# Kernel optimization log

Measured on AMD Instinct MI355X. Metric: run time of the kernel, lower is better.

Reference implementation:

```python
import jax, jax.numpy as jnp
import numpy as np

IN, OUT, RANK = 4096, 4096, 8
ALPHA = 8.0

def _quantize_int8(x):
    # row-wise symmetric int8 quantization (matches torch _quantize_int8)
    scale = jnp.max(jnp.abs(x), axis=1) / 127.0              # [rows]
    q = jnp.round(x / jnp.clip(scale, 1e-12)[:, None]).astype(jnp.int8)
    return q, scale


def setup_inputs() -> dict:
    key = jax.random.key(0)
    k_x, k_w, k_a, k_b = jax.random.split(key, 4)
    x = jax.random.normal(k_x, (8192, IN), dtype=jnp.float32)
    # simulate quantizing a pretrained fp32 weight [OUT, IN]
    w = jax.random.normal(k_w, (OUT, IN), dtype=jnp.float32) * 0.02
    w_scale = jnp.max(jnp.abs(w), axis=1) / 127.0
    weight_i8 = jnp.round(w / jnp.clip(w_scale, 1e-12)[:, None]).astype(jnp.int8)
    weight_scale = w_scale.astype(jnp.float32)               # [OUT]
    # LoRA params (lora_b random instead of zeros so output is nontrivial)
    lora_a = jax.random.normal(k_a, (RANK, IN), dtype=jnp.float32) * (1.0 / np.sqrt(IN))
    lora_b = jax.random.normal(k_b, (OUT, RANK), dtype=jnp.float32) * 0.02
    return {"x": x, "weight_i8": weight_i8, "weight_scale": weight_scale,
            "lora_a": lora_a, "lora_b": lora_b}


def reference(x, weight_i8, weight_scale, lora_a, lora_b):
    # quantize_act=True path: int8 activation quant + int8 GEMM (int32 accum) + dequant
    x_i8, x_scale = _quantize_int8(x)                         # [T, IN] int8, [T]
    out_i32 = jnp.matmul(x_i8, weight_i8.T, preferred_element_type=jnp.int32)  # [T, OUT]
    out = out_i32.astype(jnp.float32) * x_scale[:, None] * weight_scale[None, :]
    # LoRA low-rank add: x @ A^T @ B^T * (alpha / rank)
    out = out + (x @ lora_a.T) @ lora_b.T * (ALPHA / RANK)
    return out
```

## Files before the change

### kernel.cpp

```cpp
#include <hip/hip_runtime.h>
#include <stdint.h>

#define T_DIM   8192
#define IN_DIM  4096
#define OUT_DIM 4096
#define RANK    8

typedef int v4i __attribute__((ext_vector_type(4)));

__device__ __forceinline__ void async_copy16(const void* g, void* l) {
  __builtin_amdgcn_global_load_lds(
      (const __attribute__((address_space(1))) void*)g,
      (__attribute__((address_space(3))) void*)l, 16, 0, 0);
}

#define PW_BLOCKS 16384
#define QX_BLOCKS 8192
#define PREP_BLOCKS (PW_BLOCKS + QX_BLOCKS)

__global__ __launch_bounds__(256) void prep(
    const int* __restrict__ w32,
    const float* __restrict__ x,
    const float* __restrict__ lora_a,
    int8_t* __restrict__ w8,
    int8_t* __restrict__ x_i8,
    float* __restrict__ x_scale,
    float* __restrict__ xa)
{
  const int b = blockIdx.x;
  const int tid = threadIdx.x;
  __shared__ float red[4];
  __shared__ float redx[4][RANK];

  if (b < PW_BLOCKS) {
    const int idx = b * 256 + tid;
    const int4 v = ((const int4*)w32)[idx];
    char4 q;
    q.x = (signed char)v.x; q.y = (signed char)v.y;
    q.z = (signed char)v.z; q.w = (signed char)v.w;
    ((char4*)w8)[idx] = q;
    return;
  }

  const int row = b - PW_BLOCKS;
  const float4* xr = (const float4*)(x + (size_t)row * IN_DIM);
  float4 xv[4];
#pragma unroll
  for (int c = 0; c < 4; ++c) xv[c] = xr[c * 256 + tid];

  float am = 0.f;
#pragma unroll
  for (int c = 0; c < 4; ++c)
    am = fmaxf(am, fmaxf(fmaxf(fabsf(xv[c].x), fabsf(xv[c].y)),
                         fmaxf(fabsf(xv[c].z), fabsf(xv[c].w))));
#pragma unroll
  for (int off = 32; off > 0; off >>= 1)
    am = fmaxf(am, __shfl_xor(am, off, 64));
  if ((tid & 63) == 0) red[tid >> 6] = am;

  float dot[RANK];
#pragma unroll
  for (int r = 0; r < RANK; ++r) {
    const float4* ar = (const float4*)(lora_a + (size_t)r * IN_DIM);
    float s = 0.f;
#pragma unroll
    for (int c = 0; c < 4; ++c) {
      const float4 a = ar[c * 256 + tid];
      s += xv[c].x * a.x + xv[c].y * a.y + xv[c].z * a.z + xv[c].w * a.w;
    }
    dot[r] = s;
  }
#pragma unroll
  for (int off = 32; off > 0; off >>= 1) {
#pragma unroll
    for (int r = 0; r < RANK; ++r)
      dot[r] += __shfl_xor(dot[r], off, 64);
  }
  if ((tid & 63) == 0) {
#pragma unroll
    for (int r = 0; r < RANK; ++r) redx[tid >> 6][r] = dot[r];
  }
  __syncthreads();

  const float amax = fmaxf(fmaxf(red[0], red[1]), fmaxf(red[2], red[3]));
  const float scale = amax * (1.0f / 127.0f);
  const float inv = 1.0f / fmaxf(scale, 1e-12f);
  char4* qout = (char4*)(x_i8 + (size_t)row * IN_DIM);
#pragma unroll
  for (int c = 0; c < 4; ++c) {
    char4 q;
    q.x = (signed char)(int)rintf(xv[c].x * inv);
    q.y = (signed char)(int)rintf(xv[c].y * inv);
    q.z = (signed char)(int)rintf(xv[c].z * inv);
    q.w = (signed char)(int)rintf(xv[c].w * inv);
    qout[c * 256 + tid] = q;
  }
  if (tid == 0) x_scale[row] = scale;
  if (tid < RANK)
    xa[(size_t)row * RANK + tid] =
        redx[0][tid] + redx[1][tid] + redx[2][tid] + redx[3][tid];
}

#define SYNC(n) do {                                      \
    asm volatile("s_waitcnt vmcnt(" #n ")" ::: "memory"); \
    __builtin_amdgcn_s_barrier();                         \
    __builtin_amdgcn_sched_barrier(0);                    \
  } while (0)

__device__ __forceinline__ void stage_tile(const int8_t* aSrc, const int8_t* bSrc,
                                           int8_t* Lbuf, int ldsOff) {
  async_copy16(aSrc,                          Lbuf + ldsOff);
  async_copy16(aSrc + (size_t)128 * IN_DIM,   Lbuf + 8192 + ldsOff);
  async_copy16(bSrc,                          Lbuf + 16384 + ldsOff);
  async_copy16(bSrc + (size_t)128 * IN_DIM,   Lbuf + 16384 + 8192 + ldsOff);
}

__device__ __forceinline__ void compute_tile(const int8_t* Lbuf, int aOff, int bOff,
                                             v4i (&acc)[8][4]) {
  const int8_t* La = Lbuf;
  const int8_t* Lb = Lbuf + 16384;
  v4i aF[8], bF[4];
#pragma unroll
  for (int i = 0; i < 8; ++i) aF[i] = *(const v4i*)(La + aOff + i * 1024);
#pragma unroll
  for (int j = 0; j < 4; ++j) bF[j] = *(const v4i*)(Lb + bOff + j * 1024);
  __builtin_amdgcn_s_setprio(1);
#pragma unroll
  for (int i = 0; i < 8; ++i)
#pragma unroll
    for (int j = 0; j < 4; ++j)
      acc[i][j] = __builtin_amdgcn_mfma_i32_16x16x64_i8(aF[i], bF[j], acc[i][j], 0, 0, 0);
  __builtin_amdgcn_s_setprio(0);
}

__global__ __launch_bounds__(512, 2) void gemm256_i8(
    const int8_t* __restrict__ A,
    const int8_t* __restrict__ B,
    const float* __restrict__ x_scale,
    const float* __restrict__ w_scale,
    const float* __restrict__ xa,
    const float* __restrict__ lora_b,
    float* __restrict__ out)
{
  __shared__ __align__(16) int8_t smem[3 * 32768];
  const int tid = threadIdx.x;

  const int orig = blockIdx.x;
  const int wgid = ((orig & 7) << 6) | (orig >> 3);
  const int by = wgid >> 4;
  const int bx = wgid & 15;
  const size_t arow0 = (size_t)by * 256;
  const size_t brow0 = (size_t)bx * 256;

  const int r_l = tid >> 2;
  const int qsw = ((tid & 3) ^ ((r_l >> 1) & 3)) << 4;
  const int8_t* aSrc = A + (arow0 + r_l) * IN_DIM + qsw;
  const int8_t* bSrc = B + (brow0 + r_l) * IN_DIM + qsw;
  const int ldsOff = tid << 4;

  const int lane = tid & 63;
  const int wave = tid >> 6;
  const int wr = wave >> 2, wc = wave & 3;
  const int m16 = lane & 15, quad = lane >> 4;
  const int sw = (quad ^ ((m16 >> 1) & 3)) << 4;
  const int aOff = (wr * 128 + m16) * 64 + sw;
  const int bOff = (wc * 64 + m16) * 64 + sw;

  v4i acc[8][4];
  const v4i vz = {0, 0, 0, 0};
#pragma unroll
  for (int i = 0; i < 8; ++i)
#pragma unroll
    for (int j = 0; j < 4; ++j) acc[i][j] = vz;

  stage_tile(aSrc, bSrc, smem, ldsOff);
  stage_tile(aSrc + 64, bSrc + 64, smem + 32768, ldsOff);

#pragma unroll 1
  for (int t = 0; t < 60; t += 3) {
    SYNC(4);
    stage_tile(aSrc + (t + 2) * 64, bSrc + (t + 2) * 64, smem + 2 * 32768, ldsOff);
    compute_tile(smem, aOff, bOff, acc);
    SYNC(4);
    stage_tile(aSrc + (t + 3) * 64, bSrc + (t + 3) * 64, smem, ldsOff);
    compute_tile(smem + 32768, aOff, bOff, acc);
    SYNC(4);
    stage_tile(aSrc + (t + 4) * 64, bSrc + (t + 4) * 64, smem + 32768, ldsOff);
    compute_tile(smem + 2 * 32768, aOff, bOff, acc);
  }
  SYNC(4);
  stage_tile(aSrc + 62 * 64, bSrc + 62 * 64, smem + 2 * 32768, ldsOff);
  compute_tile(smem, aOff, bOff, acc);
  SYNC(4);
  stage_tile(aSrc + 63 * 64, bSrc + 63 * 64, smem, ldsOff);
  compute_tile(smem + 32768, aOff, bOff, acc);
  SYNC(4);
  compute_tile(smem + 2 * 32768, aOff, bOff, acc);
  asm volatile("s_waitcnt vmcnt(0)" ::: "memory");
  __builtin_amdgcn_s_barrier();
  __builtin_amdgcn_sched_barrier(0);
  compute_tile(smem, aOff, bOff, acc);

  __syncthreads();
  float* fs   = (float*)smem;
  float* xs_s = fs;
  float* ws_s = fs + 256;
  float* xa_s = fs + 512;
  float* lb_s = fs + 2560;
  if (tid < 256) xs_s[tid] = x_scale[arow0 + tid];
  else           ws_s[tid - 256] = w_scale[brow0 + (tid - 256)];
  ((float4*)xa_s)[tid] = ((const float4*)(xa + arow0 * RANK))[tid];
  ((float4*)lb_s)[tid] = ((const float4*)(lora_b + brow0 * RANK))[tid];
  __syncthreads();

  float wscv[4];
  float4 lb0[4], lb1[4];
  int cols[4];
#pragma unroll
  for (int j = 0; j < 4; ++j) {
    const int c = wc * 64 + j * 16 + m16;
    cols[j] = c;
    wscv[j] = ws_s[c];
    lb0[j] = *(const float4*)(lb_s + c * RANK);
    lb1[j] = *(const float4*)(lb_s + c * RANK + 4);
  }
#pragma unroll
  for (int i = 0; i < 8; ++i) {
#pragma unroll
    for (int reg = 0; reg < 4; ++reg) {
      const int r = wr * 128 + i * 16 + quad * 4 + reg;
      const float xsc = xs_s[r];
      const float4 xa0 = *(const float4*)(xa_s + r * RANK);
      const float4 xa1 = *(const float4*)(xa_s + r * RANK + 4);
      float* orow = out + (arow0 + (size_t)r) * OUT_DIM + brow0;
#pragma unroll
      for (int j = 0; j < 4; ++j) {
        float v = (float)acc[i][j][reg] * xsc * wscv[j];
        v += xa0.x * lb0[j].x + xa0.y * lb0[j].y + xa0.z * lb0[j].z + xa0.w * lb0[j].w +
             xa1.x * lb1[j].x + xa1.y * lb1[j].y + xa1.z * lb1[j].z + xa1.w * lb1[j].w;
        orow[cols[j]] = v;
      }
    }
  }
}

extern "C" void kernel_launch(void* const* d_in, const int* in_sizes, int n_in,
                              void* d_out, int out_size, void* d_ws, size_t ws_size,
                              hipStream_t stream) {
  const float* x       = (const float*)d_in[0];
  const int*   w_i32   = (const int*)d_in[1];
  const float* w_scale = (const float*)d_in[2];
  const float* lora_a  = (const float*)d_in[3];
  const float* lora_b  = (const float*)d_in[4];
  float* out = (float*)d_out;

  int8_t* x_i8    = (int8_t*)d_ws;
  int8_t* w8      = x_i8 + (size_t)T_DIM * IN_DIM;
  float*  x_scale = (float*)(w8 + (size_t)OUT_DIM * IN_DIM);
  float*  xa      = x_scale + T_DIM;

  prep<<<PREP_BLOCKS, 256, 0, stream>>>(w_i32, x, lora_a, w8, x_i8, x_scale, xa);
  gemm256_i8<<<(T_DIM / 256) * (OUT_DIM / 256), 512, 0, stream>>>(
      x_i8, w8, x_scale, w_scale, xa, lora_b, out);
}
```

Measured before the change: 407.9 us.

## Restructure int8 GEMM mainloop into double-buffered 128-K stages with interleaved loads

Replaces the triple-buffered 64-K LDS pipeline with a double-buffered scheme where each stage covers 128 K elements (two 64-K subtiles), using 128 KB of shared memory. Global-to-LDS async copies for the next stage are spread across eight sub-phases, each interleaved with a slice of fragment loads and MFMAs. This aims to overlap memory traffic with compute more finely and halve loop iterations. The cost is more barriers per iteration and larger LDS, which may limit occupancy to one block per CU despite launch bounds of two. The last iteration redundantly reloads the final K slice into the unused buffer.

```diff
diff --git a/kernel.cpp b/kernel.cpp
--- a/kernel.cpp
+++ b/kernel.cpp
@@ -101,38 +101,6 @@
         redx[0][tid] + redx[1][tid] + redx[2][tid] + redx[3][tid];
 }
 
-#define SYNC(n) do {                                      \
-    asm volatile("s_waitcnt vmcnt(" #n ")" ::: "memory"); \
-    __builtin_amdgcn_s_barrier();                         \
-    __builtin_amdgcn_sched_barrier(0);                    \
-  } while (0)
-
-__device__ __forceinline__ void stage_tile(const int8_t* aSrc, const int8_t* bSrc,
-                                           int8_t* Lbuf, int ldsOff) {
-  async_copy16(aSrc,                          Lbuf + ldsOff);
-  async_copy16(aSrc + (size_t)128 * IN_DIM,   Lbuf + 8192 + ldsOff);
-  async_copy16(bSrc,                          Lbuf + 16384 + ldsOff);
-  async_copy16(bSrc + (size_t)128 * IN_DIM,   Lbuf + 16384 + 8192 + ldsOff);
-}
-
-__device__ __forceinline__ void compute_tile(const int8_t* Lbuf, int aOff, int bOff,
-                                             v4i (&acc)[8][4]) {
-  const int8_t* La = Lbuf;
-  const int8_t* Lb = Lbuf + 16384;
-  v4i aF[8], bF[4];
-#pragma unroll
-  for (int i = 0; i < 8; ++i) aF[i] = *(const v4i*)(La + aOff + i * 1024);
-#pragma unroll
-  for (int j = 0; j < 4; ++j) bF[j] = *(const v4i*)(Lb + bOff + j * 1024);
-  __builtin_amdgcn_s_setprio(1);
-#pragma unroll
-  for (int i = 0; i < 8; ++i)
-#pragma unroll
-    for (int j = 0; j < 4; ++j)
-      acc[i][j] = __builtin_amdgcn_mfma_i32_16x16x64_i8(aF[i], bF[j], acc[i][j], 0, 0, 0);
-  __builtin_amdgcn_s_setprio(0);
-}
-
 __global__ __launch_bounds__(512, 2) void gemm256_i8(
     const int8_t* __restrict__ A,
     const int8_t* __restrict__ B,
@@ -142,7 +110,7 @@
     const float* __restrict__ lora_b,
     float* __restrict__ out)
 {
-  __shared__ __align__(16) int8_t smem[3 * 32768];
+  __shared__ __align__(16) int8_t smem[2 * 65536];
   const int tid = threadIdx.x;
 
   const int orig = blockIdx.x;
@@ -164,7 +132,7 @@
   const int m16 = lane & 15, quad = lane >> 4;
   const int sw = (quad ^ ((m16 >> 1) & 3)) << 4;
   const int aOff = (wr * 128 + m16) * 64 + sw;
-  const int bOff = (wc * 64 + m16) * 64 + sw;
+  const int bOff = 32768 + (wc * 64 + m16) * 64 + sw;
 
   v4i acc[8][4];
   const v4i vz = {0, 0, 0, 0};
@@ -173,34 +141,58 @@
 #pragma unroll
     for (int j = 0; j < 4; ++j) acc[i][j] = vz;
 
-  stage_tile(aSrc, bSrc, smem, ldsOff);
-  stage_tile(aSrc + 64, bSrc + 64, smem + 32768, ldsOff);
-
-#pragma unroll 1
-  for (int t = 0; t < 60; t += 3) {
-    SYNC(4);
-    stage_tile(aSrc + (t + 2) * 64, bSrc + (t + 2) * 64, smem + 2 * 32768, ldsOff);
-    compute_tile(smem, aOff, bOff, acc);
-    SYNC(4);
-    stage_tile(aSrc + (t + 3) * 64, bSrc + (t + 3) * 64, smem, ldsOff);
-    compute_tile(smem + 32768, aOff, bOff, acc);
-    SYNC(4);
-    stage_tile(aSrc + (t + 4) * 64, bSrc + (t + 4) * 64, smem + 32768, ldsOff);
-    compute_tile(smem + 2 * 32768, aOff, bOff, acc);
-  }
-  SYNC(4);
-  stage_tile(aSrc + 62 * 64, bSrc + 62 * 64, smem + 2 * 32768, ldsOff);
-  compute_tile(smem, aOff, bOff, acc);
-  SYNC(4);
-  stage_tile(aSrc + 63 * 64, bSrc + 63 * 64, smem, ldsOff);
-  compute_tile(smem + 32768, aOff, bOff, acc);
-  SYNC(4);
-  compute_tile(smem + 2 * 32768, aOff, bOff, acc);
-  asm volatile("s_waitcnt vmcnt(0)" ::: "memory");
+#pragma unroll
+  for (int p = 0; p < 8; ++p) {
+    const int kts = p >> 2, isB = (p >> 1) & 1, g = p & 1;
+    const int8_t* src = (isB ? bSrc : aSrc) + kts * 64 + (size_t)g * 128 * IN_DIM;
+    async_copy16(src, smem + isB * 32768 + kts * 16384 + g * 8192 + ldsOff);
+  }
+  asm volatile("s_waitcnt vmcnt(4)" ::: "memory");
   __builtin_amdgcn_s_barrier();
   __builtin_amdgcn_sched_barrier(0);
-  compute_tile(smem, aOff, bOff, acc);
-
+
+#pragma unroll 1
+  for (int it = 0; it < 32; ++it) {
+    const int8_t* Lcur = smem + (it & 1) * 65536;
+    int8_t* Lnxt = smem + ((it & 1) ^ 1) * 65536;
+    const int ks = (it < 31 ? it + 1 : 31) * 128;
+    v4i bF[4];
+#pragma unroll
+    for (int p = 0; p < 8; ++p) {
+      const int kt = p >> 2;
+      const int i0 = (p & 3) * 2;
+      if ((p & 3) == 0) {
+#pragma unroll
+        for (int j = 0; j < 4; ++j)
+          bF[j] = *(const v4i*)(Lcur + kt * 16384 + bOff + j * 1024);
+      }
+      const v4i aF0 = *(const v4i*)(Lcur + kt * 16384 + aOff + i0 * 1024);
+      const v4i aF1 = *(const v4i*)(Lcur + kt * 16384 + aOff + (i0 + 1) * 1024);
+      {
+        const int kts = p >> 2, isB = (p >> 1) & 1, g = p & 1;
+        const int8_t* src =
+            (isB ? bSrc : aSrc) + ks + kts * 64 + (size_t)g * 128 * IN_DIM;
+        async_copy16(src, Lnxt + isB * 32768 + kts * 16384 + g * 8192 + ldsOff);
+      }
+      __builtin_amdgcn_s_barrier();
+      asm volatile("s_waitcnt lgkmcnt(0)" ::: "memory");
+      __builtin_amdgcn_sched_barrier(0);
+      __builtin_amdgcn_s_setprio(1);
+#pragma unroll
+      for (int j = 0; j < 4; ++j)
+        acc[i0][j] = __builtin_amdgcn_mfma_i32_16x16x64_i8(aF0, bF[j], acc[i0][j], 0, 0, 0);
+#pragma unroll
+      for (int j = 0; j < 4; ++j)
+        acc[i0 + 1][j] = __builtin_amdgcn_mfma_i32_16x16x64_i8(aF1, bF[j], acc[i0 + 1][j], 0, 0, 0);
+      __builtin_amdgcn_s_setprio(0);
+      if ((p & 3) == 3)
+        asm volatile("s_waitcnt vmcnt(4)" ::: "memory");
+      __builtin_amdgcn_s_barrier();
+      __builtin_amdgcn_sched_barrier(0);
+    }
+  }
+
+  asm volatile("s_waitcnt vmcnt(0) lgkmcnt(0)" ::: "memory");
   __syncthreads();
   float* fs   = (float*)smem;
   float* xs_s = fs;
```

Result: no change. 408.8 us (+0.2%).

## Double-buffer LDS fragment reads in int8 GEMM and split prep into batched kernels

Applied to the files above, without the earlier changes.

The GEMM main loop now prefetches the next tile's LDS fragments into registers while the MFMA cluster runs on the current fragments. This hides LDS read latency behind matrix math, at the cost of more registers; the launch-bounds occupancy hint of 2 is dropped. The prep kernel is split into a weight-pack kernel and an activation-quant kernel that handles 4 rows per block, so each lora_a load is reused across those rows. Redundant tail stages re-load tile 63 rather than branching.

```diff
diff --git a/kernel.cpp b/kernel.cpp
--- a/kernel.cpp
+++ b/kernel.cpp
@@ -14,126 +14,147 @@
       (__attribute__((address_space(3))) void*)l, 16, 0, 0);
 }
 
-#define PW_BLOCKS 16384
-#define QX_BLOCKS 8192
-#define PREP_BLOCKS (PW_BLOCKS + QX_BLOCKS)
-
-__global__ __launch_bounds__(256) void prep(
-    const int* __restrict__ w32,
-    const float* __restrict__ x,
-    const float* __restrict__ lora_a,
-    int8_t* __restrict__ w8,
-    int8_t* __restrict__ x_i8,
-    float* __restrict__ x_scale,
+__global__ __launch_bounds__(256) void pack_w(
+    const int* __restrict__ w32, int8_t* __restrict__ w8)
+{
+  const int idx = blockIdx.x * 256 + threadIdx.x;
+  const int4 v = ((const int4*)w32)[idx];
+  char4 q;
+  q.x = (signed char)v.x; q.y = (signed char)v.y;
+  q.z = (signed char)v.z; q.w = (signed char)v.w;
+  ((char4*)w8)[idx] = q;
+}
+
+#define QROWS 4
+__global__ __launch_bounds__(256) void quant_x(
+    const float* __restrict__ x, const float* __restrict__ lora_a,
+    int8_t* __restrict__ x_i8, float* __restrict__ x_scale,
     float* __restrict__ xa)
 {
-  const int b = blockIdx.x;
   const int tid = threadIdx.x;
-  __shared__ float red[4];
-  __shared__ float redx[4][RANK];
-
-  if (b < PW_BLOCKS) {
-    const int idx = b * 256 + tid;
-    const int4 v = ((const int4*)w32)[idx];
-    char4 q;
-    q.x = (signed char)v.x; q.y = (signed char)v.y;
-    q.z = (signed char)v.z; q.w = (signed char)v.w;
-    ((char4*)w8)[idx] = q;
-    return;
-  }
-
-  const int row = b - PW_BLOCKS;
-  const float4* xr = (const float4*)(x + (size_t)row * IN_DIM);
-  float4 xv[4];
-#pragma unroll
-  for (int c = 0; c < 4; ++c) xv[c] = xr[c * 256 + tid];
-
-  float am = 0.f;
-#pragma unroll
-  for (int c = 0; c < 4; ++c)
-    am = fmaxf(am, fmaxf(fmaxf(fabsf(xv[c].x), fabsf(xv[c].y)),
-                         fmaxf(fabsf(xv[c].z), fabsf(xv[c].w))));
+  const int wave = tid >> 6;
+  const size_t row0 = (size_t)blockIdx.x * QROWS;
+  __shared__ float redm[4][QROWS];
+  __shared__ float redd[4][QROWS][RANK];
+
+  const float4* xr = (const float4*)(x + row0 * IN_DIM);
+  float4 xv[QROWS][4];
+#pragma unroll
+  for (int r = 0; r < QROWS; ++r)
+#pragma unroll
+    for (int c = 0; c < 4; ++c)
+      xv[r][c] = xr[r * 1024 + c * 256 + tid];
+
+  float am[QROWS];
+#pragma unroll
+  for (int r = 0; r < QROWS; ++r) {
+    float m = 0.f;
+#pragma unroll
+    for (int c = 0; c < 4; ++c)
+      m = fmaxf(m, fmaxf(fmaxf(fabsf(xv[r][c].x), fabsf(xv[r][c].y)),
+                         fmaxf(fabsf(xv[r][c].z), fabsf(xv[r][c].w))));
+    am[r] = m;
+  }
 #pragma unroll
   for (int off = 32; off > 0; off >>= 1)
-    am = fmaxf(am, __shfl_xor(am, off, 64));
-  if ((tid & 63) == 0) red[tid >> 6] = am;
-
-  float dot[RANK];
-#pragma unroll
-  for (int r = 0; r < RANK; ++r) {
-    const float4* ar = (const float4*)(lora_a + (size_t)r * IN_DIM);
-    float s = 0.f;
+#pragma unroll
+    for (int r = 0; r < QROWS; ++r)
+      am[r] = fmaxf(am[r], __shfl_xor(am[r], off, 64));
+  if ((tid & 63) == 0)
+#pragma unroll
+    for (int r = 0; r < QROWS; ++r) redm[wave][r] = am[r];
+
+  float dot[QROWS][RANK];
+#pragma unroll
+  for (int rk = 0; rk < RANK; ++rk) {
+    const float4* ar = (const float4*)(lora_a + (size_t)rk * IN_DIM);
+    float4 av[4];
+#pragma unroll
+    for (int c = 0; c < 4; ++c) av[c] = ar[c * 256 + tid];
+#pragma unroll
+    for (int r = 0; r < QROWS; ++r) {
+      float s = 0.f;
+#pragma unroll
+      for (int c = 0; c < 4; ++c)
+        s += xv[r][c].x * av[c].x + xv[r][c].y * av[c].y +
+             xv[r][c].z * av[c].z + xv[r][c].w * av[c].w;
+      dot[r][rk] = s;
+    }
+  }
+#pragma unroll
+  for (int off = 32; off > 0; off >>= 1)
+#pragma unroll
+    for (int r = 0; r < QROWS; ++r)
+#pragma unroll
+      for (int rk = 0; rk < RANK; ++rk)
+        dot[r][rk] += __shfl_xor(dot[r][rk], off, 64);
+  if ((tid & 63) == 0)
+#pragma unroll
+    for (int r = 0; r < QROWS; ++r)
+#pragma unroll
+      for (int rk = 0; rk < RANK; ++rk) redd[wave][r][rk] = dot[r][rk];
+  __syncthreads();
+
+#pragma unroll
+  for (int r = 0; r < QROWS; ++r) {
+    const float amax = fmaxf(fmaxf(redm[0][r], redm[1][r]),
+                             fmaxf(redm[2][r], redm[3][r]));
+    const float scale = amax * (1.0f / 127.0f);
+    const float inv = 1.0f / fmaxf(scale, 1e-12f);
+    char4* qout = (char4*)(x_i8 + (row0 + r) * IN_DIM);
 #pragma unroll
     for (int c = 0; c < 4; ++c) {
-      const float4 a = ar[c * 256 + tid];
-      s += xv[c].x * a.x + xv[c].y * a.y + xv[c].z * a.z + xv[c].w * a.w;
-    }
-    dot[r] = s;
-  }
-#pragma unroll
-  for (int off = 32; off > 0; off >>= 1) {
-#pragma unroll
-    for (int r = 0; r < RANK; ++r)
-      dot[r] += __shfl_xor(dot[r], off, 64);
-  }
-  if ((tid & 63) == 0) {
-#pragma unroll
-    for (int r = 0; r < RANK; ++r) redx[tid >> 6][r] = dot[r];
-  }
-  __syncthreads();
-
-  const float amax = fmaxf(fmaxf(red[0], red[1]), fmaxf(red[2], red[3]));
-  const float scale = amax * (1.0f / 127.0f);
-  const float inv = 1.0f / fmaxf(scale, 1e-12f);
-  char4* qout = (char4*)(x_i8 + (size_t)row * IN_DIM);
-#pragma unroll
-  for (int c = 0; c < 4; ++c) {
-    char4 q;
-    q.x = (signed char)(int)rintf(xv[c].x * inv);
-    q.y = (signed char)(int)rintf(xv[c].y * inv);
-    q.z = (signed char)(int)rintf(xv[c].z * inv);
-    q.w = (signed char)(int)rintf(xv[c].w * inv);
-    qout[c * 256 + tid] = q;
-  }
-  if (tid == 0) x_scale[row] = scale;
-  if (tid < RANK)
-    xa[(size_t)row * RANK + tid] =
-        redx[0][tid] + redx[1][tid] + redx[2][tid] + redx[3][tid];
-}
-
-#define SYNC(n) do {                                      \
-    asm volatile("s_waitcnt vmcnt(" #n ")" ::: "memory"); \
-    __builtin_amdgcn_s_barrier();                         \
-    __builtin_amdgcn_sched_barrier(0);                    \
-  } while (0)
+      char4 q;
+      q.x = (signed char)(int)rintf(xv[r][c].x * inv);
+      q.y = (signed char)(int)rintf(xv[r][c].y * inv);
+      q.z = (signed char)(int)rintf(xv[r][c].z * inv);
+      q.w = (signed char)(int)rintf(xv[r][c].w * inv);
+      qout[c * 256 + tid] = q;
+    }
+    if (tid == 0) x_scale[row0 + r] = scale;
+  }
+  if (tid < QROWS * RANK) {
+    const int r = tid >> 3, rk = tid & 7;
+    xa[(row0 + r) * RANK + rk] =
+        redd[0][r][rk] + redd[1][r][rk] + redd[2][r][rk] + redd[3][r][rk];
+  }
+}
 
 __device__ __forceinline__ void stage_tile(const int8_t* aSrc, const int8_t* bSrc,
                                            int8_t* Lbuf, int ldsOff) {
   async_copy16(aSrc,                          Lbuf + ldsOff);
   async_copy16(aSrc + (size_t)128 * IN_DIM,   Lbuf + 8192 + ldsOff);
   async_copy16(bSrc,                          Lbuf + 16384 + ldsOff);
-  async_copy16(bSrc + (size_t)128 * IN_DIM,   Lbuf + 16384 + 8192 + ldsOff);
-}
-
-__device__ __forceinline__ void compute_tile(const int8_t* Lbuf, int aOff, int bOff,
+  async_copy16(bSrc + (size_t)128 * IN_DIM,   Lbuf + 24576 + ldsOff);
+}
+
+__device__ __forceinline__ void read_frags(const int8_t* base, int aOff, int bOff,
+                                           v4i (&fa)[8], v4i (&fb)[4]) {
+#pragma unroll
+  for (int i = 0; i < 8; ++i) fa[i] = *(const v4i*)(base + aOff + i * 1024);
+#pragma unroll
+  for (int j = 0; j < 4; ++j) fb[j] = *(const v4i*)(base + 16384 + bOff + j * 1024);
+}
+
+__device__ __forceinline__ void mfma_cluster(const v4i (&fa)[8], const v4i (&fb)[4],
                                              v4i (&acc)[8][4]) {
-  const int8_t* La = Lbuf;
-  const int8_t* Lb = Lbuf + 16384;
-  v4i aF[8], bF[4];
-#pragma unroll
-  for (int i = 0; i < 8; ++i) aF[i] = *(const v4i*)(La + aOff + i * 1024);
-#pragma unroll
-  for (int j = 0; j < 4; ++j) bF[j] = *(const v4i*)(Lb + bOff + j * 1024);
   __builtin_amdgcn_s_setprio(1);
 #pragma unroll
   for (int i = 0; i < 8; ++i)
 #pragma unroll
     for (int j = 0; j < 4; ++j)
-      acc[i][j] = __builtin_amdgcn_mfma_i32_16x16x64_i8(aF[i], bF[j], acc[i][j], 0, 0, 0);
+      acc[i][j] = __builtin_amdgcn_mfma_i32_16x16x64_i8(fa[i], fb[j], acc[i][j], 0, 0, 0);
   __builtin_amdgcn_s_setprio(0);
 }
 
-__global__ __launch_bounds__(512, 2) void gemm256_i8(
+#define KSYNC() do {                                                   \
+    asm volatile("s_waitcnt vmcnt(4) lgkmcnt(0)" ::: "memory");        \
+    __builtin_amdgcn_sched_barrier(0);                                 \
+    __builtin_amdgcn_s_barrier();                                      \
+    __builtin_amdgcn_sched_barrier(0);                                 \
+  } while (0)
+
+__global__ __launch_bounds__(512) void gemm256_i8(
     const int8_t* __restrict__ A,
     const int8_t* __restrict__ B,
     const float* __restrict__ x_scale,
@@ -173,34 +194,42 @@
 #pragma unroll
     for (int j = 0; j < 4; ++j) acc[i][j] = vz;
 
-  stage_tile(aSrc, bSrc, smem, ldsOff);
-  stage_tile(aSrc + 64, bSrc + 64, smem + 32768, ldsOff);
-
-#pragma unroll 1
-  for (int t = 0; t < 60; t += 3) {
-    SYNC(4);
-    stage_tile(aSrc + (t + 2) * 64, bSrc + (t + 2) * 64, smem + 2 * 32768, ldsOff);
-    compute_tile(smem, aOff, bOff, acc);
-    SYNC(4);
-    stage_tile(aSrc + (t + 3) * 64, bSrc + (t + 3) * 64, smem, ldsOff);
-    compute_tile(smem + 32768, aOff, bOff, acc);
-    SYNC(4);
-    stage_tile(aSrc + (t + 4) * 64, bSrc + (t + 4) * 64, smem + 32768, ldsOff);
-    compute_tile(smem + 2 * 32768, aOff, bOff, acc);
-  }
-  SYNC(4);
-  stage_tile(aSrc + 62 * 64, bSrc + 62 * 64, smem + 2 * 32768, ldsOff);
-  compute_tile(smem, aOff, bOff, acc);
-  SYNC(4);
-  stage_tile(aSrc + 63 * 64, bSrc + 63 * 64, smem, ldsOff);
-  compute_tile(smem + 32768, aOff, bOff, acc);
-  SYNC(4);
-  compute_tile(smem + 2 * 32768, aOff, bOff, acc);
-  asm volatile("s_waitcnt vmcnt(0)" ::: "memory");
+  v4i fa0[8], fb0[4], fa1[8], fb1[4];
+
+  stage_tile(aSrc,       bSrc,       (int8_t*)smem,          ldsOff);
+  stage_tile(aSrc + 64,  bSrc + 64,  (int8_t*)smem + 32768,  ldsOff);
+  stage_tile(aSrc + 128, bSrc + 128, (int8_t*)smem + 65536,  ldsOff);
+  asm volatile("s_waitcnt vmcnt(8)" ::: "memory");
+  __builtin_amdgcn_sched_barrier(0);
   __builtin_amdgcn_s_barrier();
   __builtin_amdgcn_sched_barrier(0);
-  compute_tile(smem, aOff, bOff, acc);
-
+  read_frags((const int8_t*)smem, aOff, bOff, fa0, fb0);
+
+  int sb = 0;
+  int rb = 32768;
+#pragma unroll 1
+  for (int t = 0; t < 64; t += 2) {
+    KSYNC();
+    {
+      const int ks = (t + 3 < 64 ? t + 3 : 63) * 64;
+      stage_tile(aSrc + ks, bSrc + ks, (int8_t*)smem + sb, ldsOff);
+      read_frags((const int8_t*)smem + rb, aOff, bOff, fa1, fb1);
+      mfma_cluster(fa0, fb0, acc);
+    }
+    sb += 32768; if (sb == 98304) sb = 0;
+    rb += 32768; if (rb == 98304) rb = 0;
+    KSYNC();
+    {
+      const int ks = (t + 4 < 64 ? t + 4 : 63) * 64;
+      stage_tile(aSrc + ks, bSrc + ks, (int8_t*)smem + sb, ldsOff);
+      read_frags((const int8_t*)smem + rb, aOff, bOff, fa0, fb0);
+      mfma_cluster(fa1, fb1, acc);
+    }
+    sb += 32768; if (sb == 98304) sb = 0;
+    rb += 32768; if (rb == 98304) rb = 0;
+  }
+
+  asm volatile("s_waitcnt vmcnt(0) lgkmcnt(0)" ::: "memory");
   __syncthreads();
   float* fs   = (float*)smem;
   float* xs_s = fs;
@@ -259,7 +288,8 @@
   float*  x_scale = (float*)(w8 + (size_t)OUT_DIM * IN_DIM);
   float*  xa      = x_scale + T_DIM;
 
-  prep<<<PREP_BLOCKS, 256, 0, stream>>>(w_i32, x, lora_a, w8, x_i8, x_scale, xa);
+  pack_w<<<(OUT_DIM * IN_DIM / 4) / 256, 256, 0, stream>>>(w_i32, w8);
+  quant_x<<<T_DIM / QROWS, 256, 0, stream>>>(x, lora_a, x_i8, x_scale, xa);
   gemm256_i8<<<(T_DIM / 256) * (OUT_DIM / 256), 512, 0, stream>>>(
       x_i8, w8, x_scale, w_scale, xa, lora_b, out);
 }
```

Result: no change. 414.8 us (+1.7%).
